# Optimization experiments

Measured on AMD Instinct MI355X. Metric: run time of the kernel, lower is better.

## Reference

```python
import jax, jax.numpy as jnp
import numpy as np


def setup_inputs() -> dict:
    key = jax.random.key(0)
    feature = jax.random.normal(key, (16, 32, 48, 48, 48), dtype=jnp.float32)
    return {"feature": feature}


def reference(feature):
    # feature: [B, C, X, Y, Z]
    B, C, X, Y, Z = feature.shape
    f32 = feature.dtype
    sum_num = B * C * X * Y * Z
    mgr = feature.mean()  # global mean over the whole batch tensor
    sq = feature * feature  # [B,C,X,Y,Z]

    # ---- per-(sample, region) argmax location (first occurrence, matching the
    #      strict '>' scan in get_max_index) ----
    flat = feature.reshape(B, C, X * Y * Z)
    am = jnp.argmax(flat, axis=-1)  # [B,C] int
    mx = (am // (Y * Z)).astype(f32)
    rem = am % (Y * Z)
    my = (rem // Z).astype(f32)
    mz = (rem % Z).astype(f32)

    ii = jnp.arange(X, dtype=f32)
    jj = jnp.arange(Y, dtype=f32)
    kk = jnp.arange(Z, dtype=f32)
    dx2 = (mx[:, :, None] - ii) ** 2  # [B,C,X]
    dy2 = (my[:, :, None] - jj) ** 2  # [B,C,Y]
    dz2 = (mz[:, :, None] - kk) ** 2  # [B,C,Z]

    # NOTE: faithful to the original parenthesization bug —
    # dis += r^2 * (dx^2 + dy^2) + dz^2   (the dz^2 term is NOT scaled by r^2)
    dxy = dx2[:, :, :, None] + dy2[:, :, None, :]  # [B,C,X,Y]
    dis_loss = jnp.einsum('bcxyz,bcxy->', sq, dxy) + (X * Y) * dz2.sum()

    # ---- exclude-self channel max per voxel via top-2 along channels ----
    xt = jnp.moveaxis(feature, 1, -1)  # [B,X,Y,Z,C]
    v, idx = jax.lax.top_k(xt, 2)  # [B,X,Y,Z,2]
    c = jnp.arange(C)
    # if channel c holds the (first) max, the exclude-self max is the 2nd value
    max_others = jnp.where(c == idx[..., 0:1], v[..., 1:2], v[..., 0:1])  # [B,X,Y,Z,C]
    max_others = jnp.moveaxis(max_others, -1, 1)  # [B,C,X,Y,Z]

    div_loss = (sq * (max_others - mgr) ** 2).sum()

    dis_loss = (dis_loss / sum_num).reshape(1)
    div_loss = (div_loss / sum_num).reshape(1)
    return (dis_loss, div_loss)
```

## Files before the change

kernel.cpp:

```cpp
#include <hip/hip_runtime.h>

#define NB 16
#define NC 32
#define NBC (NB*NC)
#define NX 48
#define NY 48
#define NZ 48
#define YZ (NY*NZ)
#define XYZ (NX*NY*NZ)
#define Q (XYZ/4)
#define SUM_NUM 56623104.0
#define K2_PER_B 108
#define K2_BLOCKS (NB*K2_PER_B)

struct Ws {
  int   amax[NBC];
  float vsum[NBC];
  float S0[NBC];
  float Sx[NBC];
  float Sy[NBC];
  float Sq2[NBC];
  float pA[K2_BLOCKS];
  float pB[K2_BLOCKS];
};

__global__ __launch_bounds__(1024) void k_moments(const float* __restrict__ f,
                                                  Ws* __restrict__ ws) {
  const int bc = blockIdx.x;
  const float4* __restrict__ p = reinterpret_cast<const float4*>(f + (size_t)bc * XYZ);
  const int t = threadIdx.x;
  float bmax = -3.402823466e38f;
  int bidx = 0;
  float vs = 0.f, s0 = 0.f, sx = 0.f, sy = 0.f, sq2 = 0.f;
  for (int i = t; i < Q; i += 1024) {
    const float4 v = p[i];
    const int base = i << 2;
    const int xi = i / 576;
    const int yi = (i / 12) % 48;
    const float xf = (float)xi, yf = (float)yi;
    const float sq = (v.x*v.x + v.y*v.y) + (v.z*v.z + v.w*v.w);
    vs += (v.x + v.y) + (v.z + v.w);
    s0 += sq;
    sx  = fmaf(sq, xf, sx);
    sy  = fmaf(sq, yf, sy);
    sq2 = fmaf(sq, fmaf(xf, xf, yf*yf), sq2);
    if (v.x > bmax) { bmax = v.x; bidx = base;   }
    if (v.y > bmax) { bmax = v.y; bidx = base+1; }
    if (v.z > bmax) { bmax = v.z; bidx = base+2; }
    if (v.w > bmax) { bmax = v.w; bidx = base+3; }
  }
  for (int off = 32; off > 0; off >>= 1) {
    vs  += __shfl_down(vs,  off);
    s0  += __shfl_down(s0,  off);
    sx  += __shfl_down(sx,  off);
    sy  += __shfl_down(sy,  off);
    sq2 += __shfl_down(sq2, off);
    const float ov = __shfl_down(bmax, off);
    const int   oi = __shfl_down(bidx, off);
    if (ov > bmax || (ov == bmax && oi < bidx)) { bmax = ov; bidx = oi; }
  }
  __shared__ float svs[16], ss0[16], ssx[16], ssy[16], ssq2[16], smx[16];
  __shared__ int   sbi[16];
  const int wid = t >> 6;
  if ((t & 63) == 0) {
    svs[wid] = vs; ss0[wid] = s0; ssx[wid] = sx; ssy[wid] = sy;
    ssq2[wid] = sq2; smx[wid] = bmax; sbi[wid] = bidx;
  }
  __syncthreads();
  if (t == 0) {
    for (int w = 1; w < 16; w++) {
      vs += svs[w]; s0 += ss0[w]; sx += ssx[w]; sy += ssy[w]; sq2 += ssq2[w];
      if (smx[w] > bmax || (smx[w] == bmax && sbi[w] < bidx)) { bmax = smx[w]; bidx = sbi[w]; }
    }
    ws->amax[bc] = bidx;
    ws->vsum[bc] = vs;
    ws->S0[bc]   = s0;
    ws->Sx[bc]   = sx;
    ws->Sy[bc]   = sy;
    ws->Sq2[bc]  = sq2;
  }
}

__global__ __launch_bounds__(256) void k_top2(const float* __restrict__ f,
                                              Ws* __restrict__ ws) {
  const int b    = blockIdx.x / K2_PER_B;
  const int sblk = blockIdx.x % K2_PER_B;
  const int t = threadIdx.x;
  const float4* __restrict__ p =
      reinterpret_cast<const float4*>(f + (size_t)b * NC * XYZ) + (sblk * 256 + t);

  const float NEG = -3.402823466e38f;
  float4 m1 = make_float4(NEG,NEG,NEG,NEG);
  float4 m2 = make_float4(NEG,NEG,NEG,NEG);
  float4 s0 = make_float4(0.f,0.f,0.f,0.f);

  #pragma unroll 8
  for (int c = 0; c < NC; c++) {
    const float4 v = p[(size_t)c * Q];
    s0.x = fmaf(v.x, v.x, s0.x);
    s0.y = fmaf(v.y, v.y, s0.y);
    s0.z = fmaf(v.z, v.z, s0.z);
    s0.w = fmaf(v.w, v.w, s0.w);
    if (v.x > m1.x) { m2.x = m1.x; m1.x = v.x; } else if (v.x > m2.x) m2.x = v.x;
    if (v.y > m1.y) { m2.y = m1.y; m1.y = v.y; } else if (v.y > m2.y) m2.y = v.y;
    if (v.z > m1.z) { m2.z = m1.z; m1.z = v.z; } else if (v.z > m2.z) m2.z = v.z;
    if (v.w > m1.w) { m2.w = m1.w; m1.w = v.w; } else if (v.w > m2.w) m2.w = v.w;
  }

  float A = 0.f, Bv = 0.f;
  {
    float q1, rest;
    q1 = m1.x*m1.x; rest = s0.x - q1;
    A  = fmaf(q1, rest, A);  A  = fmaf(m2.x*m2.x, q1, A);
    Bv = fmaf(m1.x, rest, Bv); Bv = fmaf(m2.x, q1, Bv);
    q1 = m1.y*m1.y; rest = s0.y - q1;
    A  = fmaf(q1, rest, A);  A  = fmaf(m2.y*m2.y, q1, A);
    Bv = fmaf(m1.y, rest, Bv); Bv = fmaf(m2.y, q1, Bv);
    q1 = m1.z*m1.z; rest = s0.z - q1;
    A  = fmaf(q1, rest, A);  A  = fmaf(m2.z*m2.z, q1, A);
    Bv = fmaf(m1.z, rest, Bv); Bv = fmaf(m2.z, q1, Bv);
    q1 = m1.w*m1.w; rest = s0.w - q1;
    A  = fmaf(q1, rest, A);  A  = fmaf(m2.w*m2.w, q1, A);
    Bv = fmaf(m1.w, rest, Bv); Bv = fmaf(m2.w, q1, Bv);
  }

  for (int off = 32; off > 0; off >>= 1) {
    A  += __shfl_down(A,  off);
    Bv += __shfl_down(Bv, off);
  }
  __shared__ float rA[4], rB[4];
  const int wid = t >> 6;
  if ((t & 63) == 0) { rA[wid] = A; rB[wid] = Bv; }
  __syncthreads();
  if (t == 0) {
    ws->pA[blockIdx.x] = (rA[0] + rA[1]) + (rA[2] + rA[3]);
    ws->pB[blockIdx.x] = (rB[0] + rB[1]) + (rB[2] + rB[3]);
  }
}

__global__ __launch_bounds__(512) void k_fin(const Ws* __restrict__ ws,
                                             float* __restrict__ out) {
  const int t = threadIdx.x;
  double dis, vs, c0, a = 0.0, bb = 0.0;
  {
    const int idx = ws->amax[t];
    const double mx = (double)(idx / YZ);
    const double my = (double)((idx / NZ) % NY);
    const double mz = (double)(idx % NZ);
    const double S0 = ws->S0[t], Sx = ws->Sx[t], Sy = ws->Sy[t], Sq2 = ws->Sq2[t];
    dis = Sq2 - 2.0*mx*Sx - 2.0*my*Sy + (mx*mx + my*my)*S0
        + 2304.0 * (48.0*mz*mz - 2256.0*mz + 35720.0);
    vs = ws->vsum[t];
    c0 = S0;
  }
  for (int i = t; i < K2_BLOCKS; i += 512) { a += ws->pA[i]; bb += ws->pB[i]; }

  for (int off = 32; off > 0; off >>= 1) {
    dis += __shfl_down(dis, off);
    vs  += __shfl_down(vs,  off);
    c0  += __shfl_down(c0,  off);
    a   += __shfl_down(a,   off);
    bb  += __shfl_down(bb,  off);
  }
  __shared__ double sd[8][5];
  const int wid = t >> 6;
  if ((t & 63) == 0) { sd[wid][0]=dis; sd[wid][1]=vs; sd[wid][2]=c0; sd[wid][3]=a; sd[wid][4]=bb; }
  __syncthreads();
  if (t == 0) {
    for (int w = 1; w < 8; w++) {
      dis += sd[w][0]; vs += sd[w][1]; c0 += sd[w][2]; a += sd[w][3]; bb += sd[w][4];
    }
    const double mgr = vs / SUM_NUM;
    out[0] = (float)(dis / SUM_NUM);
    out[1] = (float)((a - 2.0*mgr*bb + mgr*mgr*c0) / SUM_NUM);
  }
}

extern "C" void kernel_launch(void* const* d_in, const int* in_sizes, int n_in,
                              void* d_out, int out_size, void* d_ws, size_t ws_size,
                              hipStream_t stream) {
  const float* f = (const float*)d_in[0];
  Ws* ws = (Ws*)d_ws;
  float* out = (float*)d_out;
  hipLaunchKernelGGL(k_moments, dim3(NBC),       dim3(1024), 0, stream, f, ws);
  hipLaunchKernelGGL(k_top2,    dim3(K2_BLOCKS), dim3(256),  0, stream, f, ws);
  hipLaunchKernelGGL(k_fin,     dim3(1),         dim3(512),  0, stream, ws, out);
}
```

Before: 77.17 us.

## Fuse moments and top-2 kernels into one heterogeneous launch per batch

Merges the per-channel moments/argmax kernel and the cross-channel top-2 kernel into a single launch. Each batch gets 140 blocks: 32 run the moments pass (now 256 threads each) and 108 run the top-2 pass, interleaved so both passes can overlap and the same batch's data may be reused in L2. The argmax inner loop now takes a local max over the float4 before comparing with the running max. This removes one launch boundary and the serialization between the two passes, but moments blocks now do 4x more work per thread than the top-2 blocks, which can cause tail imbalance.

```diff
diff --git a/kernel.cpp b/kernel.cpp
--- a/kernel.cpp
+++ b/kernel.cpp
@@ -1,140 +1,134 @@
 #include <hip/hip_runtime.h>
+#include <cfloat>
+#include <climits>
 
 #define NB 16
 #define NC 32
 #define NBC (NB*NC)
-#define NX 48
+#define NZ 48
 #define NY 48
-#define NZ 48
-#define YZ (NY*NZ)
-#define XYZ (NX*NY*NZ)
+#define YZ 2304
+#define XYZ 110592
 #define Q (XYZ/4)
 #define SUM_NUM 56623104.0
-#define K2_PER_B 108
-#define K2_BLOCKS (NB*K2_PER_B)
+#define NBLK_B 108
+#define K2_BLOCKS (NB*NBLK_B)
+#define RPS 140
+#define GRID (NB*RPS)
 
 struct Ws {
   int   amax[NBC];
-  float vsum[NBC];
-  float S0[NBC];
-  float Sx[NBC];
-  float Sy[NBC];
-  float Sq2[NBC];
-  float pA[K2_BLOCKS];
-  float pB[K2_BLOCKS];
+  float vsum[NBC], S0[NBC], Sx[NBC], Sy[NBC], Sq2[NBC];
+  float pA[K2_BLOCKS], pB[K2_BLOCKS];
 };
 
-__global__ __launch_bounds__(1024) void k_moments(const float* __restrict__ f,
-                                                  Ws* __restrict__ ws) {
-  const int bc = blockIdx.x;
-  const float4* __restrict__ p = reinterpret_cast<const float4*>(f + (size_t)bc * XYZ);
+#define TOP2(m1, m2, x) do { \
+    if ((x) > (m1)) { (m2) = (m1); (m1) = (x); } \
+    else if ((x) > (m2)) (m2) = (x); \
+  } while (0)
+
+__global__ __launch_bounds__(256) void k_all(const float* __restrict__ f,
+                                             Ws* __restrict__ ws) {
+  const int b = blockIdx.x / RPS;
+  const int r = blockIdx.x - b * RPS;
   const int t = threadIdx.x;
-  float bmax = -3.402823466e38f;
-  int bidx = 0;
-  float vs = 0.f, s0 = 0.f, sx = 0.f, sy = 0.f, sq2 = 0.f;
-  for (int i = t; i < Q; i += 1024) {
-    const float4 v = p[i];
-    const int base = i << 2;
-    const int xi = i / 576;
-    const int yi = (i / 12) % 48;
-    const float xf = (float)xi, yf = (float)yi;
-    const float sq = (v.x*v.x + v.y*v.y) + (v.z*v.z + v.w*v.w);
-    vs += (v.x + v.y) + (v.z + v.w);
-    s0 += sq;
-    sx  = fmaf(sq, xf, sx);
-    sy  = fmaf(sq, yf, sy);
-    sq2 = fmaf(sq, fmaf(xf, xf, yf*yf), sq2);
-    if (v.x > bmax) { bmax = v.x; bidx = base;   }
-    if (v.y > bmax) { bmax = v.y; bidx = base+1; }
-    if (v.z > bmax) { bmax = v.z; bidx = base+2; }
-    if (v.w > bmax) { bmax = v.w; bidx = base+3; }
-  }
-  for (int off = 32; off > 0; off >>= 1) {
-    vs  += __shfl_down(vs,  off);
-    s0  += __shfl_down(s0,  off);
-    sx  += __shfl_down(sx,  off);
-    sy  += __shfl_down(sy,  off);
-    sq2 += __shfl_down(sq2, off);
-    const float ov = __shfl_down(bmax, off);
-    const int   oi = __shfl_down(bidx, off);
-    if (ov > bmax || (ov == bmax && oi < bidx)) { bmax = ov; bidx = oi; }
-  }
-  __shared__ float svs[16], ss0[16], ssx[16], ssy[16], ssq2[16], smx[16];
-  __shared__ int   sbi[16];
-  const int wid = t >> 6;
-  if ((t & 63) == 0) {
-    svs[wid] = vs; ss0[wid] = s0; ssx[wid] = sx; ssy[wid] = sy;
-    ssq2[wid] = sq2; smx[wid] = bmax; sbi[wid] = bidx;
-  }
-  __syncthreads();
-  if (t == 0) {
-    for (int w = 1; w < 16; w++) {
-      vs += svs[w]; s0 += ss0[w]; sx += ssx[w]; sy += ssy[w]; sq2 += ssq2[w];
-      if (smx[w] > bmax || (smx[w] == bmax && sbi[w] < bidx)) { bmax = smx[w]; bidx = sbi[w]; }
+  const int w = t >> 6, l = t & 63;
+  const int fA  = (32 * r) / RPS;
+  const int fA1 = (32 * (r + 1)) / RPS;
+
+  if (fA1 > fA) {
+    const int bc = b * NC + fA;
+    const float4* __restrict__ p = reinterpret_cast<const float4*>(f + (size_t)bc * XYZ);
+    float bmax = -FLT_MAX; int bidx = 0;
+    float vs = 0.f, s0 = 0.f, sx = 0.f, sy = 0.f, sq2 = 0.f;
+#pragma unroll 4
+    for (int i = t; i < Q; i += 256) {
+      const float4 v = p[i];
+      const int base = i << 2;
+      const float xf = (float)(i / 576);
+      const float yf = (float)((i / 12) % 48);
+      const float sq = (v.x*v.x + v.y*v.y) + (v.z*v.z + v.w*v.w);
+      vs += (v.x + v.y) + (v.z + v.w);
+      s0 += sq;
+      sx  = fmaf(sq, xf, sx);
+      sy  = fmaf(sq, yf, sy);
+      sq2 = fmaf(sq, fmaf(xf, xf, yf*yf), sq2);
+      float m = v.x; int e = 0;
+      if (v.y > m) { m = v.y; e = 1; }
+      if (v.z > m) { m = v.z; e = 2; }
+      if (v.w > m) { m = v.w; e = 3; }
+      if (m > bmax) { bmax = m; bidx = base + e; }
     }
-    ws->amax[bc] = bidx;
-    ws->vsum[bc] = vs;
-    ws->S0[bc]   = s0;
-    ws->Sx[bc]   = sx;
-    ws->Sy[bc]   = sy;
-    ws->Sq2[bc]  = sq2;
-  }
-}
-
-__global__ __launch_bounds__(256) void k_top2(const float* __restrict__ f,
-                                              Ws* __restrict__ ws) {
-  const int b    = blockIdx.x / K2_PER_B;
-  const int sblk = blockIdx.x % K2_PER_B;
-  const int t = threadIdx.x;
-  const float4* __restrict__ p =
-      reinterpret_cast<const float4*>(f + (size_t)b * NC * XYZ) + (sblk * 256 + t);
-
-  const float NEG = -3.402823466e38f;
-  float4 m1 = make_float4(NEG,NEG,NEG,NEG);
-  float4 m2 = make_float4(NEG,NEG,NEG,NEG);
-  float4 s0 = make_float4(0.f,0.f,0.f,0.f);
-
-  #pragma unroll 8
-  for (int c = 0; c < NC; c++) {
-    const float4 v = p[(size_t)c * Q];
-    s0.x = fmaf(v.x, v.x, s0.x);
-    s0.y = fmaf(v.y, v.y, s0.y);
-    s0.z = fmaf(v.z, v.z, s0.z);
-    s0.w = fmaf(v.w, v.w, s0.w);
-    if (v.x > m1.x) { m2.x = m1.x; m1.x = v.x; } else if (v.x > m2.x) m2.x = v.x;
-    if (v.y > m1.y) { m2.y = m1.y; m1.y = v.y; } else if (v.y > m2.y) m2.y = v.y;
-    if (v.z > m1.z) { m2.z = m1.z; m1.z = v.z; } else if (v.z > m2.z) m2.z = v.z;
-    if (v.w > m1.w) { m2.w = m1.w; m1.w = v.w; } else if (v.w > m2.w) m2.w = v.w;
-  }
-
-  float A = 0.f, Bv = 0.f;
-  {
-    float q1, rest;
-    q1 = m1.x*m1.x; rest = s0.x - q1;
-    A  = fmaf(q1, rest, A);  A  = fmaf(m2.x*m2.x, q1, A);
-    Bv = fmaf(m1.x, rest, Bv); Bv = fmaf(m2.x, q1, Bv);
-    q1 = m1.y*m1.y; rest = s0.y - q1;
-    A  = fmaf(q1, rest, A);  A  = fmaf(m2.y*m2.y, q1, A);
-    Bv = fmaf(m1.y, rest, Bv); Bv = fmaf(m2.y, q1, Bv);
-    q1 = m1.z*m1.z; rest = s0.z - q1;
-    A  = fmaf(q1, rest, A);  A  = fmaf(m2.z*m2.z, q1, A);
-    Bv = fmaf(m1.z, rest, Bv); Bv = fmaf(m2.z, q1, Bv);
-    q1 = m1.w*m1.w; rest = s0.w - q1;
-    A  = fmaf(q1, rest, A);  A  = fmaf(m2.w*m2.w, q1, A);
-    Bv = fmaf(m1.w, rest, Bv); Bv = fmaf(m2.w, q1, Bv);
-  }
-
-  for (int off = 32; off > 0; off >>= 1) {
-    A  += __shfl_down(A,  off);
-    Bv += __shfl_down(Bv, off);
-  }
-  __shared__ float rA[4], rB[4];
-  const int wid = t >> 6;
-  if ((t & 63) == 0) { rA[wid] = A; rB[wid] = Bv; }
-  __syncthreads();
-  if (t == 0) {
-    ws->pA[blockIdx.x] = (rA[0] + rA[1]) + (rA[2] + rA[3]);
-    ws->pB[blockIdx.x] = (rB[0] + rB[1]) + (rB[2] + rB[3]);
+    for (int off = 32; off > 0; off >>= 1) {
+      vs  += __shfl_down(vs,  off);
+      s0  += __shfl_down(s0,  off);
+      sx  += __shfl_down(sx,  off);
+      sy  += __shfl_down(sy,  off);
+      sq2 += __shfl_down(sq2, off);
+      const float ov = __shfl_down(bmax, off);
+      const int   oi = __shfl_down(bidx, off);
+      if (ov > bmax || (ov == bmax && oi < bidx)) { bmax = ov; bidx = oi; }
+    }
+    __shared__ float svs[4], ss0[4], ssx[4], ssy[4], ssq2[4], smx[4];
+    __shared__ int   sbi[4];
+    if (l == 0) { svs[w]=vs; ss0[w]=s0; ssx[w]=sx; ssy[w]=sy; ssq2[w]=sq2;
+                  smx[w]=bmax; sbi[w]=bidx; }
+    __syncthreads();
+    if (t == 0) {
+      for (int q = 1; q < 4; ++q) {
+        vs += svs[q]; s0 += ss0[q]; sx += ssx[q]; sy += ssy[q]; sq2 += ssq2[q];
+        if (smx[q] > bmax || (smx[q] == bmax && sbi[q] < bidx)) { bmax = smx[q]; bidx = sbi[q]; }
+      }
+      ws->amax[bc] = bidx; ws->vsum[bc] = vs; ws->S0[bc] = s0;
+      ws->Sx[bc] = sx; ws->Sy[bc] = sy; ws->Sq2[bc] = sq2;
+    }
+  } else {
+    const int sblk = r - fA1;
+    const float4* __restrict__ p =
+        reinterpret_cast<const float4*>(f + (size_t)b * NC * XYZ) + (sblk * 256 + t);
+    float m1x=-FLT_MAX, m1y=-FLT_MAX, m1z=-FLT_MAX, m1w=-FLT_MAX;
+    float m2x=-FLT_MAX, m2y=-FLT_MAX, m2z=-FLT_MAX, m2w=-FLT_MAX;
+    float4 s0 = make_float4(0.f, 0.f, 0.f, 0.f);
+#pragma unroll 8
+    for (int c = 0; c < NC; ++c) {
+      const float4 v = p[(size_t)c * Q];
+      s0.x = fmaf(v.x, v.x, s0.x);
+      s0.y = fmaf(v.y, v.y, s0.y);
+      s0.z = fmaf(v.z, v.z, s0.z);
+      s0.w = fmaf(v.w, v.w, s0.w);
+      TOP2(m1x, m2x, v.x);
+      TOP2(m1y, m2y, v.y);
+      TOP2(m1z, m2z, v.z);
+      TOP2(m1w, m2w, v.w);
+    }
+    float A = 0.f, Bv = 0.f;
+    {
+      float q1, rest;
+      q1 = m1x*m1x; rest = s0.x - q1;
+      A = fmaf(q1, rest, A); A = fmaf(m2x*m2x, q1, A);
+      Bv = fmaf(m1x, rest, Bv); Bv = fmaf(m2x, q1, Bv);
+      q1 = m1y*m1y; rest = s0.y - q1;
+      A = fmaf(q1, rest, A); A = fmaf(m2y*m2y, q1, A);
+      Bv = fmaf(m1y, rest, Bv); Bv = fmaf(m2y, q1, Bv);
+      q1 = m1z*m1z; rest = s0.z - q1;
+      A = fmaf(q1, rest, A); A = fmaf(m2z*m2z, q1, A);
+      Bv = fmaf(m1z, rest, Bv); Bv = fmaf(m2z, q1, Bv);
+      q1 = m1w*m1w; rest = s0.w - q1;
+      A = fmaf(q1, rest, A); A = fmaf(m2w*m2w, q1, A);
+      Bv = fmaf(m1w, rest, Bv); Bv = fmaf(m2w, q1, Bv);
+    }
+    for (int off = 32; off > 0; off >>= 1) {
+      A  += __shfl_down(A,  off);
+      Bv += __shfl_down(Bv, off);
+    }
+    __shared__ float rA[4], rB[4];
+    if (l == 0) { rA[w] = A; rB[w] = Bv; }
+    __syncthreads();
+    if (t == 0) {
+      const int pidx = b * NBLK_B + sblk;
+      ws->pA[pidx] = (rA[0] + rA[1]) + (rA[2] + rA[3]);
+      ws->pB[pidx] = (rB[0] + rB[1]) + (rB[2] + rB[3]);
+    }
   }
 }
 
@@ -167,8 +161,8 @@
   if ((t & 63) == 0) { sd[wid][0]=dis; sd[wid][1]=vs; sd[wid][2]=c0; sd[wid][3]=a; sd[wid][4]=bb; }
   __syncthreads();
   if (t == 0) {
-    for (int w = 1; w < 8; w++) {
-      dis += sd[w][0]; vs += sd[w][1]; c0 += sd[w][2]; a += sd[w][3]; bb += sd[w][4];
+    for (int q = 1; q < 8; ++q) {
+      dis += sd[q][0]; vs += sd[q][1]; c0 += sd[q][2]; a += sd[q][3]; bb += sd[q][4];
     }
     const double mgr = vs / SUM_NUM;
     out[0] = (float)(dis / SUM_NUM);
@@ -182,7 +176,6 @@
   const float* f = (const float*)d_in[0];
   Ws* ws = (Ws*)d_ws;
   float* out = (float*)d_out;
-  hipLaunchKernelGGL(k_moments, dim3(NBC),       dim3(1024), 0, stream, f, ws);
-  hipLaunchKernelGGL(k_top2,    dim3(K2_BLOCKS), dim3(256),  0, stream, f, ws);
-  hipLaunchKernelGGL(k_fin,     dim3(1),         dim3(512),  0, stream, ws, out);
+  hipLaunchKernelGGL(k_all, dim3(GRID), dim3(256), 0, stream, f, ws);
+  hipLaunchKernelGGL(k_fin, dim3(1),    dim3(512), 0, stream, ws, out);
 }
```

New measurement: 74.78 us (median of 2 runs). 1.03x faster.
